# Optimization experiments

Hardware: AMD Instinct MI355X
Metric: run time of the kernel (lower is better)

## Reference

```python
import jax, jax.numpy as jnp
import numpy as np

B, C, H, W = 8, 64, 256, 256
S = 512          # style_dim
K = 3            # modulated conv kernel
LRELU_SLOPE = 0.2
FUSED_SCALE = float(np.sqrt(2.0))
LIN_SCALE = 1.0 / float(np.sqrt(S))          # EqualLinear scale
CONV_SCALE = 1.0 / float(np.sqrt(C * K * K)) # ModulatedConv2d scale


def setup_inputs() -> dict:
    key = jax.random.key(0)
    ks = jax.random.split(key, 8)
    kaiming = float(np.sqrt(2.0 / (C * 9)))  # torch Conv2d default-ish init scale
    return {
        "x": jax.random.normal(ks[0], (B, C, H, W), jnp.float32),
        "style": jax.random.normal(ks[1], (B, S), jnp.float32),
        # bottleneck_IR block 1 (bn=False -> Identity norms, shortcut=identity)
        "w1a": jax.random.normal(ks[2], (C, C, 3, 3), jnp.float32) * kaiming,
        "alpha1": jnp.full((C,), 0.25, jnp.float32),
        "w1b": jax.random.normal(ks[3], (C, C, 3, 3), jnp.float32) * kaiming,
        # bottleneck_IR block 2
        "w2a": jax.random.normal(ks[4], (C, C, 3, 3), jnp.float32) * kaiming,
        "alpha2": jnp.full((C,), 0.25, jnp.float32),
        "w2b": jax.random.normal(ks[5], (C, C, 3, 3), jnp.float32) * kaiming,
        # ModulatedConv2d: EqualLinear(S->C, bias_init=1) + weight [out,in,k,k]
        "mod_w": jax.random.normal(ks[6], (C, S), jnp.float32),
        "mod_b": jnp.ones((C,), jnp.float32),
        "conv_w": jax.random.normal(ks[7], (C, C, K, K), jnp.float32),
        # FusedLeakyReLU bias
        "fused_b": jnp.zeros((C,), jnp.float32),
    }


def _conv3(x, w):
    return jax.lax.conv_general_dilated(
        x, w, (1, 1), "SAME", dimension_numbers=("NCHW", "OIHW", "NCHW"))


def _prelu(x, a):
    return jnp.where(x > 0, x, a[None, :, None, None] * x)


def _bottleneck_ir(x, wa, alpha, wb):
    # shortcut is identity (in_channel==depth, stride=1); norms are Identity (bn=False)
    return x + _conv3(_prelu(_conv3(x, wa), alpha), wb)


def reference(x, style, w1a, alpha1, w1b, w2a, alpha2, w2b,
              mod_w, mod_b, conv_w, fused_b):
    h = _bottleneck_ir(x, w1a, alpha1, w1b)
    h = _bottleneck_ir(h, w2a, alpha2, w2b)

    # ModulatedConv2d (stride 1, no up/down sample, demodulate=True)
    s = style @ (mod_w.T * LIN_SCALE) + mod_b              # [B, Cin]
    w = CONV_SCALE * conv_w[None] * s[:, None, :, None, None]  # [B, Cout, Cin, K, K]
    demod = jax.lax.rsqrt(jnp.sum(w * w, axis=(2, 3, 4)) + 1e-8)
    w = w * demod[:, :, None, None, None]

    Bn, Cin, Hh, Ww = h.shape
    out = jax.lax.conv_general_dilated(
        h.reshape(1, Bn * Cin, Hh, Ww),            # grouped-conv trick
        w.reshape(Bn * C, Cin, K, K),
        (1, 1), "SAME",
        dimension_numbers=("NCHW", "OIHW", "NCHW"),
        feature_group_count=Bn,
    ).reshape(Bn, C, Hh, Ww)

    # FusedLeakyReLU: (x + bias) -> leaky_relu(0.2) -> * sqrt(2)
    ob = out + fused_b[None, :, None, None]
    return jnp.where(ob > 0, ob, LRELU_SLOPE * ob) * FUSED_SCALE
```

## Files before the change

### kernel.cpp

```cpp
#include <hip/hip_runtime.h>
#include <hip/hip_bf16.h>
#include <math.h>

#define BB 8
#define SS 512
#define LIN_SCALE 0.044194173824159216f
#define CONV_SCALE 0.041666666666666664f
#define SQRT2 1.4142135623730951f

typedef __attribute__((ext_vector_type(8))) short short8;
typedef __attribute__((ext_vector_type(16))) float f32x16;

__device__ __forceinline__ ushort bf16h(float v) {
    unsigned u = __float_as_uint(v);
    return (ushort)((u + 0x7fffu + ((u >> 16) & 1u)) >> 16);
}
__device__ __forceinline__ void splitv(float v, ushort& h, ushort& l) {
    h = bf16h(v);
    l = bf16h(v - __uint_as_float((unsigned)h << 16));
}
__device__ __forceinline__ float b2f(ushort u) { return __uint_as_float((unsigned)u << 16); }

__global__ void zero_k(float* z) { z[threadIdx.x] = 0.f; }

__global__ __launch_bounds__(256) void tocl_k(const float* __restrict__ x,
                                              ushort* __restrict__ oH, ushort* __restrict__ oL) {
    __shared__ float tile[64][65];
    const int blk = blockIdx.x;
    const int b = blk >> 10, rem = blk & 1023;
    const int y = rem >> 2, x0 = (rem & 3) << 6;
    const int tid = threadIdx.x, lane = tid & 63, g = tid >> 6;
    const float* xb = x + ((size_t)b << 22) + (y << 8) + x0;
    #pragma unroll
    for (int i = 0; i < 16; ++i) {
        int c = i * 4 + g;
        tile[c][lane] = xb[((size_t)c << 16) + lane];
    }
    __syncthreads();
    const size_t pixbase = ((size_t)b << 16) + (y << 8) + x0;
    #pragma unroll
    for (int i = 0; i < 16; ++i) {
        int xx = i * 4 + g;
        ushort h, l; splitv(tile[lane][xx], h, l);
        size_t idx = (pixbase + xx) * 64 + lane;
        oH[idx] = h; oL[idx] = l;
    }
}

__device__ __forceinline__ void wdecode(int ii, int& cc, int& sec, int& t, int& co, int& spos, int& e) {
    cc = ii / 18432; int r1 = ii % 18432;
    sec = r1 / 9216;  int r2 = r1 % 9216;
    t = r2 / 1024;    int r3 = r2 % 1024;
    co = r3 >> 4;     int r4 = r3 & 15;
    spos = r4 >> 3;   e = r4 & 7;
}

__global__ void packw_k(const float* __restrict__ w, ushort* __restrict__ img) {
    int i = blockIdx.x * 256 + threadIdx.x;
    if (i >= 73728) return;
    int cc, sec, t, co, spos, e;
    wdecode(i, cc, sec, t, co, spos, e);
    int ci = cc * 16 + ((spos ^ ((co >> 2) & 1)) << 3) + e;
    ushort h, l; splitv(w[(co * 64 + ci) * 9 + t], h, l);
    img[i] = sec ? l : h;
}

__global__ void style_s_k(const float* __restrict__ style, const float* __restrict__ mod_w,
                          const float* __restrict__ mod_b, float* __restrict__ sbuf) {
    int tid = threadIdx.x;
    int b = tid >> 6, cin = tid & 63;
    float acc = 0.f;
    for (int j = 0; j < SS; ++j) acc += style[b * SS + j] * mod_w[cin * SS + j];
    sbuf[b * 64 + cin] = acc * LIN_SCALE + mod_b[cin];
}

__global__ void demod_k(const float* __restrict__ conv_w, const float* __restrict__ sbuf,
                        float* __restrict__ demod) {
    int tid = threadIdx.x;
    int b = tid >> 6, cout = tid & 63;
    float sum = 0.f;
    for (int cin = 0; cin < 64; ++cin) {
        float m = CONV_SCALE * sbuf[b * 64 + cin];
        const float* wp = conv_w + (cout * 64 + cin) * 9;
        #pragma unroll
        for (int k = 0; k < 9; ++k) { float v = wp[k] * m; sum += v * v; }
    }
    demod[b * 64 + cout] = 1.0f / sqrtf(sum + 1e-8f);
}

__global__ void packmod_k(const float* __restrict__ conv_w, const float* __restrict__ sbuf,
                          const float* __restrict__ demod, ushort* __restrict__ img) {
    int i = blockIdx.x * 256 + threadIdx.x;
    if (i >= 589824) return;
    int b = i / 73728, ii = i % 73728;
    int cc, sec, t, co, spos, e;
    wdecode(ii, cc, sec, t, co, spos, e);
    int ci = cc * 16 + ((spos ^ ((co >> 2) & 1)) << 3) + e;
    float v = CONV_SCALE * conv_w[(co * 64 + ci) * 9 + t] * sbuf[b * 64 + ci] * demod[b * 64 + co];
    ushort h, l; splitv(v, h, l);
    img[i] = sec ? l : h;
}

#define GLDS(gsrc, ldst) __builtin_amdgcn_global_load_lds( \
    (const __attribute__((address_space(1))) unsigned int*)(gsrc), \
    (__attribute__((address_space(3))) unsigned int*)(ldst), 16, 0, 0)

#define VWAIT(n) asm volatile("s_waitcnt vmcnt(" #n ")" ::: "memory")
#define LWAIT    asm volatile("s_waitcnt lgkmcnt(0)" ::: "memory")
#define BAR      __builtin_amdgcn_s_barrier()
#define SCB      __builtin_amdgcn_sched_barrier(0)

template <int EPI, int PERB>
__global__ __launch_bounds__(256, 2)
void mconv_k(const ushort* __restrict__ inH, const ushort* __restrict__ inL,
             const char* __restrict__ wimg, const float* __restrict__ aux,
             const ushort* __restrict__ rH, const ushort* __restrict__ rL,
             ushort* __restrict__ oH, ushort* __restrict__ oL,
             float* __restrict__ onchw, const ushort* __restrict__ zb) {
    __shared__ __align__(16) char lds[80384];
    const int tid = threadIdx.x;
    const int orig = blockIdx.x;
    const int blk = (orig & 7) * 256 + (orig >> 3);
    const int b = blk >> 8, t8 = blk & 255;
    const int y0 = (t8 >> 3) << 3, x0 = (t8 & 7) << 5;
    const int wv = tid >> 6, l = tid & 63, ln = l & 31, lh = l >> 5;

    const ushort* iaddr[5];
    #pragma unroll
    for (int r = 0; r < 5; ++r) {
        int g = r * 256 + tid;
        int isL = g >= 640;
        int gg = g - (isL ? 640 : 0);
        int p = gg >> 1, sl = gg & 1;
        int h = sl ^ ((p >> 2) & 1);
        int row = p >> 5, xi = p & 31;
        int gy = y0 - 1 + row;
        const ushort* base = isL ? inL : inH;
        iaddr[r] = ((unsigned)gy < 256u)
            ? base + ((((size_t)b << 16) + ((size_t)gy << 8) + (x0 + xi)) << 6) + (h << 3)
            : zb;
    }
    const char* wsrc = wimg + (PERB ? (size_t)b * 147456 : 0);
    const int aswz = lh ^ ((ln >> 2) & 1);
    const int aoff0 = 43520 + ln * 32 + aswz * 16;

    f32x16 acc[2][2];
    #pragma unroll
    for (int m = 0; m < 2; ++m)
        #pragma unroll
        for (int j = 0; j < 2; ++j) acc[m][j] = (f32x16)(0.0f);

#define ISSUE_I(c, bo) { _Pragma("unroll") for (int r = 0; r < 5; ++r) \
    GLDS(iaddr[r] + (c) * 16, lds + (bo) + r * 4096 + (tid & 192) * 16); }
#define ISSUE_W(c) { _Pragma("unroll") for (int r = 0; r < 9; ++r) \
    GLDS(wsrc + (c) * 36864 + r * 4096 + tid * 16, lds + 43520 + r * 4096 + (tid & 192) * 16); }
#define HALO_LD(cx, V, D) { D = 0; if (tid < 80) { \
    int hp = tid >> 2, s = tid & 3; \
    int row = hp >> 1, side = hp & 1; \
    int gy = y0 - 1 + row, gx = side ? x0 + 32 : x0 - 1; \
    int pl = s >> 1, hh = s & 1; \
    const ushort* bse = pl ? inL : inH; \
    const ushort* a = (((unsigned)gy < 256u) & ((unsigned)gx < 256u)) \
        ? bse + ((((size_t)b << 16) + ((size_t)gy << 8) + gx) << 6) + (cx) * 16 + (hh << 3) : zb; \
    V = *(const uint4*)a; \
    D = (pl ? 21120 : 20480) + (hp * 2 + hh) * 16; } }
#define HALO_WR(bo, V, D) { if (tid < 80) *(uint4*)(lds + (bo) + D) = V; }
#define COMPUTE(bo) { const char* IB = lds + (bo); \
  _Pragma("unroll") for (int dx = 0; dx < 3; ++dx) { \
    short8 cbH[4], cbL[4]; \
    _Pragma("unroll") for (int rw = 0; rw < 4; ++rw) { \
      int rr = 2 * wv + rw, xx = ln + dx; \
      int p = rr * 32 + xx - 1; \
      int offI = p * 32 + (lh ^ ((p >> 2) & 1)) * 16; \
      int hal = (xx == 0) | (xx == 33); \
      int offH = 20480 + (rr * 2 + (xx != 0)) * 32 + lh * 16; \
      int off = hal ? offH : offI; \
      int dL = hal ? 640 : 10240; \
      cbH[rw] = *(const short8*)(IB + off); \
      cbL[rw] = *(const short8*)(IB + off + dL); } \
    _Pragma("unroll") for (int dy = 0; dy < 3; ++dy) { \
      const char* WA = lds + (dy * 3 + dx) * 2048; \
      short8 aH0 = *(const short8*)(WA + aoff0); \
      short8 aH1 = *(const short8*)(WA + aoff0 + 1024); \
      short8 aL0 = *(const short8*)(WA + aoff0 + 18432); \
      short8 aL1 = *(const short8*)(WA + aoff0 + 18432 + 1024); \
      _Pragma("unroll") for (int j = 0; j < 2; ++j) { \
        acc[0][j] = __builtin_amdgcn_mfma_f32_32x32x16_bf16(aH0, cbH[j + dy], acc[0][j], 0, 0, 0); \
        acc[0][j] = __builtin_amdgcn_mfma_f32_32x32x16_bf16(aH0, cbL[j + dy], acc[0][j], 0, 0, 0); \
        acc[0][j] = __builtin_amdgcn_mfma_f32_32x32x16_bf16(aL0, cbH[j + dy], acc[0][j], 0, 0, 0); \
        acc[1][j] = __builtin_amdgcn_mfma_f32_32x32x16_bf16(aH1, cbH[j + dy], acc[1][j], 0, 0, 0); \
        acc[1][j] = __builtin_amdgcn_mfma_f32_32x32x16_bf16(aH1, cbL[j + dy], acc[1][j], 0, 0, 0); \
        acc[1][j] = __builtin_amdgcn_mfma_f32_32x32x16_bf16(aL1, cbH[j + dy], acc[1][j], 0, 0, 0); } } } }

    uint4 hv, hv2; int hd, hd2;
    HALO_LD(0, hv, hd); HALO_LD(1, hv2, hd2);
    SCB;
    ISSUE_W(0); ISSUE_I(0, 0); ISSUE_I(1, 21760);
    SCB;
    HALO_WR(0, hv, hd); HALO_WR(21760, hv2, hd2);
    SCB;
    VWAIT(5); LWAIT; BAR; SCB;
    COMPUTE(0);
    SCB; BAR;
    HALO_LD(2, hv, hd); SCB;
    ISSUE_W(1); ISSUE_I(2, 0); SCB;
    HALO_WR(0, hv, hd); SCB;
    VWAIT(5); LWAIT; BAR; SCB;
    COMPUTE(21760);
    SCB; BAR;
    HALO_LD(3, hv, hd); SCB;
    ISSUE_W(2); ISSUE_I(3, 21760); SCB;
    HALO_WR(21760, hv, hd); SCB;
    VWAIT(5); LWAIT; BAR; SCB;
    COMPUTE(0);
    SCB; BAR;
    ISSUE_W(3); SCB;
    VWAIT(0); LWAIT; BAR; SCB;
    COMPUTE(21760);
    SCB;

#undef ISSUE_I
#undef ISSUE_W
#undef HALO_LD
#undef HALO_WR
#undef COMPUTE

    #pragma unroll
    for (int m = 0; m < 2; ++m)
        #pragma unroll
        for (int j = 0; j < 2; ++j) {
            const int yo = y0 + 2 * wv + j;
            const size_t pix = ((size_t)b << 16) + ((size_t)yo << 8) + x0 + ln;
            #pragma unroll
            for (int q = 0; q < 4; ++q) {
                const int co0 = m * 32 + 8 * q + 4 * lh;
                float v0 = acc[m][j][4 * q + 0], v1 = acc[m][j][4 * q + 1];
                float v2 = acc[m][j][4 * q + 2], v3 = acc[m][j][4 * q + 3];
                if (EPI == 0) {
                    float4 al = *(const float4*)(aux + co0);
                    v0 = v0 > 0.f ? v0 : al.x * v0;
                    v1 = v1 > 0.f ? v1 : al.y * v1;
                    v2 = v2 > 0.f ? v2 : al.z * v2;
                    v3 = v3 > 0.f ? v3 : al.w * v3;
                } else if (EPI == 1) {
                    const size_t ca = pix * 64 + co0;
                    ushort4 rh = *(const ushort4*)(rH + ca);
                    ushort4 rl = *(const ushort4*)(rL + ca);
                    v0 += b2f(rh.x) + b2f(rl.x);
                    v1 += b2f(rh.y) + b2f(rl.y);
                    v2 += b2f(rh.z) + b2f(rl.z);
                    v3 += b2f(rh.w) + b2f(rl.w);
                } else {
                    float4 bi = *(const float4*)(aux + co0);
                    float ob;
                    ob = v0 + bi.x; v0 = (ob > 0.f ? ob : 0.2f * ob) * SQRT2;
                    ob = v1 + bi.y; v1 = (ob > 0.f ? ob : 0.2f * ob) * SQRT2;
                    ob = v2 + bi.z; v2 = (ob > 0.f ? ob : 0.2f * ob) * SQRT2;
                    ob = v3 + bi.w; v3 = (ob > 0.f ? ob : 0.2f * ob) * SQRT2;
                }
                if (EPI == 2) {
                    const size_t sp = ((size_t)yo << 8) + x0 + ln;
                    onchw[(((size_t)(b * 64 + co0 + 0)) << 16) + sp] = v0;
                    onchw[(((size_t)(b * 64 + co0 + 1)) << 16) + sp] = v1;
                    onchw[(((size_t)(b * 64 + co0 + 2)) << 16) + sp] = v2;
                    onchw[(((size_t)(b * 64 + co0 + 3)) << 16) + sp] = v3;
                } else {
                    ushort4 h4, l4;
                    splitv(v0, h4.x, l4.x); splitv(v1, h4.y, l4.y);
                    splitv(v2, h4.z, l4.z); splitv(v3, h4.w, l4.w);
                    const size_t ca = pix * 64 + co0;
                    *(ushort4*)(oH + ca) = h4;
                    *(ushort4*)(oL + ca) = l4;
                }
            }
        }
}

extern "C" void kernel_launch(void* const* d_in, const int* in_sizes, int n_in,
                              void* d_out, int out_size, void* d_ws, size_t ws_size,
                              hipStream_t stream) {
    const float* x       = (const float*)d_in[0];
    const float* style   = (const float*)d_in[1];
    const float* w1a     = (const float*)d_in[2];
    const float* alpha1  = (const float*)d_in[3];
    const float* w1b     = (const float*)d_in[4];
    const float* w2a     = (const float*)d_in[5];
    const float* alpha2  = (const float*)d_in[6];
    const float* w2b     = (const float*)d_in[7];
    const float* mod_w   = (const float*)d_in[8];
    const float* mod_b   = (const float*)d_in[9];
    const float* conv_w  = (const float*)d_in[10];
    const float* fused_b = (const float*)d_in[11];
    float* out = (float*)d_out;

    char* ws = (char*)d_ws;
    float*  zbf   = (float*)ws;
    float*  sbuf  = (float*)(ws + 256);
    float*  demod = (float*)(ws + 2304);
    ushort* wfix  = (ushort*)(ws + 4352);
    ushort* wmod  = (ushort*)(ws + 594176);
    char*   pl    = ws + 1774080;
    const size_t PAIRB = 134217728ull;
    const size_t PLEL  = 33554432ull;

    ushort* XPH = (ushort*)pl;             ushort* XPL = XPH + PLEL;
    ushort* PBH = (ushort*)(pl + PAIRB);   ushort* PBL = PBH + PLEL;
    ushort *PAH, *PAL;
    if (ws_size >= 1774080ull + 3 * PAIRB) {
        PAH = (ushort*)(pl + 2 * PAIRB); PAL = PAH + PLEL;
    } else {
        PAH = (ushort*)d_out; PAL = PAH + PLEL;
    }
    const ushort* zb = (const ushort*)zbf;

    hipLaunchKernelGGL(zero_k, dim3(1), dim3(64), 0, stream, zbf);
    hipLaunchKernelGGL(tocl_k, dim3(BB * 1024), dim3(256), 0, stream, x, XPH, XPL);
    hipLaunchKernelGGL(packw_k, dim3(288), dim3(256), 0, stream, w1a, wfix + 0 * 73728);
    hipLaunchKernelGGL(packw_k, dim3(288), dim3(256), 0, stream, w1b, wfix + 1 * 73728);
    hipLaunchKernelGGL(packw_k, dim3(288), dim3(256), 0, stream, w2a, wfix + 2 * 73728);
    hipLaunchKernelGGL(packw_k, dim3(288), dim3(256), 0, stream, w2b, wfix + 3 * 73728);
    hipLaunchKernelGGL(style_s_k, dim3(1), dim3(512), 0, stream, style, mod_w, mod_b, sbuf);
    hipLaunchKernelGGL(demod_k, dim3(1), dim3(512), 0, stream, conv_w, sbuf, demod);
    hipLaunchKernelGGL(packmod_k, dim3(2304), dim3(256), 0, stream, conv_w, sbuf, demod, wmod);

    const dim3 cgrid(2048), cblk(256);
    hipLaunchKernelGGL((mconv_k<0, 0>), cgrid, cblk, 0, stream,
        XPH, XPL, (const char*)(wfix + 0 * 73728), alpha1, (const ushort*)nullptr, (const ushort*)nullptr,
        PAH, PAL, (float*)nullptr, zb);
    hipLaunchKernelGGL((mconv_k<1, 0>), cgrid, cblk, 0, stream,
        PAH, PAL, (const char*)(wfix + 1 * 73728), (const float*)nullptr, XPH, XPL,
        PBH, PBL, (float*)nullptr, zb);
    hipLaunchKernelGGL((mconv_k<0, 0>), cgrid, cblk, 0, stream,
        PBH, PBL, (const char*)(wfix + 2 * 73728), alpha2, (const ushort*)nullptr, (const ushort*)nullptr,
        PAH, PAL, (float*)nullptr, zb);
    hipLaunchKernelGGL((mconv_k<1, 0>), cgrid, cblk, 0, stream,
        PAH, PAL, (const char*)(wfix + 3 * 73728), (const float*)nullptr, PBH, PBL,
        PBH, PBL, (float*)nullptr, zb);
    hipLaunchKernelGGL((mconv_k<2, 1>), cgrid, cblk, 0, stream,
        PBH, PBL, (const char*)wmod, fused_b, (const ushort*)nullptr, (const ushort*)nullptr,
        (ushort*)nullptr, (ushort*)nullptr, out, zb);
}
```

Baseline: 924.9 us.

## Load input tiles directly from global into registers, shrink LDS to weights only

Removes the LDS staging of the input activation tile and its halo. Each lane now reads its B-operand fragments straight from global memory, with bounds-checked addresses falling back to a zero buffer. LDS holds only the per-chunk weight image, so the weight layout and swizzle are reworked and LDS drops from about 80KB to 36KB. Launch bounds are raised to 3 blocks per CU for more occupancy. The cost is redundant uncoalesced global/L2 reads of overlapping pixels and no double-buffered overlap, since each chunk's weight load fully waits before compute.

```diff
diff --git a/kernel.cpp b/kernel.cpp
--- a/kernel.cpp
+++ b/kernel.cpp
@@ -47,22 +47,27 @@
     }
 }
 
-__device__ __forceinline__ void wdecode(int ii, int& cc, int& sec, int& t, int& co, int& spos, int& e) {
-    cc = ii / 18432; int r1 = ii % 18432;
-    sec = r1 / 9216;  int r2 = r1 % 9216;
-    t = r2 / 1024;    int r3 = r2 % 1024;
-    co = r3 >> 4;     int r4 = r3 & 15;
-    spos = r4 >> 3;   e = r4 & 7;
+__device__ __forceinline__ void wdecode(int i, int& cc, int& t, int& co, int& ci, int& pl) {
+    int e = i & 7;
+    int s = i >> 3;
+    cc = s / 2304;
+    int s2 = s % 2304;
+    t = s2 >> 8;
+    int co8 = s2 & 255;
+    co = co8 >> 2;
+    int sp = co8 & 3;
+    int slog = sp ^ ((co >> 1) & 3);
+    pl = slog >> 1;
+    ci = cc * 16 + (slog & 1) * 8 + e;
 }
 
 __global__ void packw_k(const float* __restrict__ w, ushort* __restrict__ img) {
     int i = blockIdx.x * 256 + threadIdx.x;
     if (i >= 73728) return;
-    int cc, sec, t, co, spos, e;
-    wdecode(i, cc, sec, t, co, spos, e);
-    int ci = cc * 16 + ((spos ^ ((co >> 2) & 1)) << 3) + e;
+    int cc, t, co, ci, pl;
+    wdecode(i, cc, t, co, ci, pl);
     ushort h, l; splitv(w[(co * 64 + ci) * 9 + t], h, l);
-    img[i] = sec ? l : h;
+    img[i] = pl ? l : h;
 }
 
 __global__ void style_s_k(const float* __restrict__ style, const float* __restrict__ mod_w,
@@ -93,31 +98,28 @@
     int i = blockIdx.x * 256 + threadIdx.x;
     if (i >= 589824) return;
     int b = i / 73728, ii = i % 73728;
-    int cc, sec, t, co, spos, e;
-    wdecode(ii, cc, sec, t, co, spos, e);
-    int ci = cc * 16 + ((spos ^ ((co >> 2) & 1)) << 3) + e;
+    int cc, t, co, ci, pl;
+    wdecode(ii, cc, t, co, ci, pl);
     float v = CONV_SCALE * conv_w[(co * 64 + ci) * 9 + t] * sbuf[b * 64 + ci] * demod[b * 64 + co];
     ushort h, l; splitv(v, h, l);
-    img[i] = sec ? l : h;
+    img[i] = pl ? l : h;
 }
 
 #define GLDS(gsrc, ldst) __builtin_amdgcn_global_load_lds( \
     (const __attribute__((address_space(1))) unsigned int*)(gsrc), \
     (__attribute__((address_space(3))) unsigned int*)(ldst), 16, 0, 0)
 
-#define VWAIT(n) asm volatile("s_waitcnt vmcnt(" #n ")" ::: "memory")
-#define LWAIT    asm volatile("s_waitcnt lgkmcnt(0)" ::: "memory")
-#define BAR      __builtin_amdgcn_s_barrier()
-#define SCB      __builtin_amdgcn_sched_barrier(0)
+#define VWAIT0 asm volatile("s_waitcnt vmcnt(0)" ::: "memory")
+#define BAR    __builtin_amdgcn_s_barrier()
 
 template <int EPI, int PERB>
-__global__ __launch_bounds__(256, 2)
+__global__ __launch_bounds__(256, 3)
 void mconv_k(const ushort* __restrict__ inH, const ushort* __restrict__ inL,
              const char* __restrict__ wimg, const float* __restrict__ aux,
              const ushort* __restrict__ rH, const ushort* __restrict__ rL,
              ushort* __restrict__ oH, ushort* __restrict__ oL,
              float* __restrict__ onchw, const ushort* __restrict__ zb) {
-    __shared__ __align__(16) char lds[80384];
+    __shared__ __align__(16) char lds[36864];
     const int tid = threadIdx.x;
     const int orig = blockIdx.x;
     const int blk = (orig & 7) * 256 + (orig >> 3);
@@ -125,24 +127,10 @@
     const int y0 = (t8 >> 3) << 3, x0 = (t8 & 7) << 5;
     const int wv = tid >> 6, l = tid & 63, ln = l & 31, lh = l >> 5;
 
-    const ushort* iaddr[5];
-    #pragma unroll
-    for (int r = 0; r < 5; ++r) {
-        int g = r * 256 + tid;
-        int isL = g >= 640;
-        int gg = g - (isL ? 640 : 0);
-        int p = gg >> 1, sl = gg & 1;
-        int h = sl ^ ((p >> 2) & 1);
-        int row = p >> 5, xi = p & 31;
-        int gy = y0 - 1 + row;
-        const ushort* base = isL ? inL : inH;
-        iaddr[r] = ((unsigned)gy < 256u)
-            ? base + ((((size_t)b << 16) + ((size_t)gy << 8) + (x0 + xi)) << 6) + (h << 3)
-            : zb;
-    }
     const char* wsrc = wimg + (PERB ? (size_t)b * 147456 : 0);
-    const int aswz = lh ^ ((ln >> 2) & 1);
-    const int aoff0 = 43520 + ln * 32 + aswz * 16;
+    const int swz = (ln >> 1) & 3;
+    const int offH = ln * 64 + ((lh ^ swz) << 4);
+    const int offL = ln * 64 + (((2 + lh) ^ swz) << 4);
 
     f32x16 acc[2][2];
     #pragma unroll
@@ -150,80 +138,51 @@
         #pragma unroll
         for (int j = 0; j < 2; ++j) acc[m][j] = (f32x16)(0.0f);
 
-#define ISSUE_I(c, bo) { _Pragma("unroll") for (int r = 0; r < 5; ++r) \
-    GLDS(iaddr[r] + (c) * 16, lds + (bo) + r * 4096 + (tid & 192) * 16); }
 #define ISSUE_W(c) { _Pragma("unroll") for (int r = 0; r < 9; ++r) \
-    GLDS(wsrc + (c) * 36864 + r * 4096 + tid * 16, lds + 43520 + r * 4096 + (tid & 192) * 16); }
-#define HALO_LD(cx, V, D) { D = 0; if (tid < 80) { \
-    int hp = tid >> 2, s = tid & 3; \
-    int row = hp >> 1, side = hp & 1; \
-    int gy = y0 - 1 + row, gx = side ? x0 + 32 : x0 - 1; \
-    int pl = s >> 1, hh = s & 1; \
-    const ushort* bse = pl ? inL : inH; \
-    const ushort* a = (((unsigned)gy < 256u) & ((unsigned)gx < 256u)) \
-        ? bse + ((((size_t)b << 16) + ((size_t)gy << 8) + gx) << 6) + (cx) * 16 + (hh << 3) : zb; \
-    V = *(const uint4*)a; \
-    D = (pl ? 21120 : 20480) + (hp * 2 + hh) * 16; } }
-#define HALO_WR(bo, V, D) { if (tid < 80) *(uint4*)(lds + (bo) + D) = V; }
-#define COMPUTE(bo) { const char* IB = lds + (bo); \
-  _Pragma("unroll") for (int dx = 0; dx < 3; ++dx) { \
-    short8 cbH[4], cbL[4]; \
-    _Pragma("unroll") for (int rw = 0; rw < 4; ++rw) { \
-      int rr = 2 * wv + rw, xx = ln + dx; \
-      int p = rr * 32 + xx - 1; \
-      int offI = p * 32 + (lh ^ ((p >> 2) & 1)) * 16; \
-      int hal = (xx == 0) | (xx == 33); \
-      int offH = 20480 + (rr * 2 + (xx != 0)) * 32 + lh * 16; \
-      int off = hal ? offH : offI; \
-      int dL = hal ? 640 : 10240; \
-      cbH[rw] = *(const short8*)(IB + off); \
-      cbL[rw] = *(const short8*)(IB + off + dL); } \
-    _Pragma("unroll") for (int dy = 0; dy < 3; ++dy) { \
-      const char* WA = lds + (dy * 3 + dx) * 2048; \
-      short8 aH0 = *(const short8*)(WA + aoff0); \
-      short8 aH1 = *(const short8*)(WA + aoff0 + 1024); \
-      short8 aL0 = *(const short8*)(WA + aoff0 + 18432); \
-      short8 aL1 = *(const short8*)(WA + aoff0 + 18432 + 1024); \
-      _Pragma("unroll") for (int j = 0; j < 2; ++j) { \
-        acc[0][j] = __builtin_amdgcn_mfma_f32_32x32x16_bf16(aH0, cbH[j + dy], acc[0][j], 0, 0, 0); \
-        acc[0][j] = __builtin_amdgcn_mfma_f32_32x32x16_bf16(aH0, cbL[j + dy], acc[0][j], 0, 0, 0); \
-        acc[0][j] = __builtin_amdgcn_mfma_f32_32x32x16_bf16(aL0, cbH[j + dy], acc[0][j], 0, 0, 0); \
-        acc[1][j] = __builtin_amdgcn_mfma_f32_32x32x16_bf16(aH1, cbH[j + dy], acc[1][j], 0, 0, 0); \
-        acc[1][j] = __builtin_amdgcn_mfma_f32_32x32x16_bf16(aH1, cbL[j + dy], acc[1][j], 0, 0, 0); \
-        acc[1][j] = __builtin_amdgcn_mfma_f32_32x32x16_bf16(aL1, cbH[j + dy], acc[1][j], 0, 0, 0); } } } }
-
-    uint4 hv, hv2; int hd, hd2;
-    HALO_LD(0, hv, hd); HALO_LD(1, hv2, hd2);
-    SCB;
-    ISSUE_W(0); ISSUE_I(0, 0); ISSUE_I(1, 21760);
-    SCB;
-    HALO_WR(0, hv, hd); HALO_WR(21760, hv2, hd2);
-    SCB;
-    VWAIT(5); LWAIT; BAR; SCB;
-    COMPUTE(0);
-    SCB; BAR;
-    HALO_LD(2, hv, hd); SCB;
-    ISSUE_W(1); ISSUE_I(2, 0); SCB;
-    HALO_WR(0, hv, hd); SCB;
-    VWAIT(5); LWAIT; BAR; SCB;
-    COMPUTE(21760);
-    SCB; BAR;
-    HALO_LD(3, hv, hd); SCB;
-    ISSUE_W(2); ISSUE_I(3, 21760); SCB;
-    HALO_WR(21760, hv, hd); SCB;
-    VWAIT(5); LWAIT; BAR; SCB;
-    COMPUTE(0);
-    SCB; BAR;
-    ISSUE_W(3); SCB;
-    VWAIT(0); LWAIT; BAR; SCB;
-    COMPUTE(21760);
-    SCB;
-
-#undef ISSUE_I
+    GLDS(wsrc + (c) * 36864 + r * 4096 + tid * 16, lds + r * 4096 + (tid & 192) * 16); }
+
+    ISSUE_W(0); VWAIT0; BAR;
+
+    #pragma unroll
+    for (int c = 0; c < 4; ++c) {
+        const int c0 = c * 16 + lh * 8;
+        #pragma unroll
+        for (int dx = 0; dx < 3; ++dx) {
+            short8 bH[4], bL[4];
+            #pragma unroll
+            for (int r = 0; r < 4; ++r) {
+                const int gy = y0 + 2 * wv - 1 + r;
+                const int gx = x0 + ln + dx - 1;
+                const bool valid = ((unsigned)gy < 256u) & ((unsigned)gx < 256u);
+                const size_t poff = ((((size_t)b << 16) + ((size_t)(gy & 255) << 8) + (gx & 255)) << 6) + c0;
+                const ushort* pH = valid ? inH + poff : zb;
+                const ushort* pL = valid ? inL + poff : zb;
+                bH[r] = *(const short8*)pH;
+                bL[r] = *(const short8*)pL;
+            }
+            #pragma unroll
+            for (int dy = 0; dy < 3; ++dy) {
+                const char* WA = lds + (dy * 3 + dx) * 4096;
+                short8 aH0 = *(const short8*)(WA + offH);
+                short8 aH1 = *(const short8*)(WA + offH + 2048);
+                short8 aL0 = *(const short8*)(WA + offL);
+                short8 aL1 = *(const short8*)(WA + offL + 2048);
+                #pragma unroll
+                for (int j = 0; j < 2; ++j) {
+                    const int r = j + dy;
+                    acc[0][j] = __builtin_amdgcn_mfma_f32_32x32x16_bf16(aH0, bH[r], acc[0][j], 0, 0, 0);
+                    acc[0][j] = __builtin_amdgcn_mfma_f32_32x32x16_bf16(aH0, bL[r], acc[0][j], 0, 0, 0);
+                    acc[0][j] = __builtin_amdgcn_mfma_f32_32x32x16_bf16(aL0, bH[r], acc[0][j], 0, 0, 0);
+                    acc[1][j] = __builtin_amdgcn_mfma_f32_32x32x16_bf16(aH1, bH[r], acc[1][j], 0, 0, 0);
+                    acc[1][j] = __builtin_amdgcn_mfma_f32_32x32x16_bf16(aH1, bL[r], acc[1][j], 0, 0, 0);
+                    acc[1][j] = __builtin_amdgcn_mfma_f32_32x32x16_bf16(aL1, bH[r], acc[1][j], 0, 0, 0);
+                }
+            }
+        }
+        BAR;
+        if (c < 3) { ISSUE_W(c + 1); VWAIT0; BAR; }
+    }
 #undef ISSUE_W
-#undef HALO_LD
-#undef HALO_WR
-#undef COMPUTE
 
     #pragma unroll
     for (int m = 0; m < 2; ++m)
```

Result: slower. 1.758 ms (+90.1%).
